# Kernel optimization log

Measured on AMD Instinct MI355X. Metric: run time of the kernel, lower is better.

## Reference

```python
import jax, jax.numpy as jnp
import numpy as np

TEMPERATURE = 0.07
BASE_TEMPERATURE = 0.07
LAMBDA_HARD = 1.0
HMAX = 1.0
EPS = 1e-8
SIGMA = 1.0  # Gaussian RBF kernel bandwidth on label differences


def setup_inputs() -> dict:
    key = jax.random.key(0)
    k1, k2 = jax.random.split(key)
    features = jax.random.normal(k1, (4096, 2, 128), dtype=jnp.float32)
    labels = jax.random.uniform(k2, (4096,), dtype=jnp.float32)
    return {"features": features, "labels": labels}


def reference(features, labels):
    bsz, n_views, dim = features.shape
    # F.normalize(features, dim=-1)
    feats = features / jnp.sqrt(jnp.sum(features * features, axis=-1, keepdims=True) + 1e-12)
    # torch.cat(torch.unbind(features, dim=1), dim=0) -> view-major stacking [N, dim]
    feats = jnp.transpose(feats, (1, 0, 2)).reshape(bsz * n_views, dim)
    lab = jnp.tile(labels.reshape(bsz, 1), (n_views, 1))  # [N, 1]
    N = bsz * n_views

    logits_mask = 1.0 - jnp.eye(N, dtype=feats.dtype)

    # kernel similarity weights w_{i,k} = K(y_i - y_k), Gaussian RBF, clamped to [0,1]
    dy = lab - lab.T                                   # [N, N]
    w = jnp.clip(jnp.exp(-(dy * dy) / (2.0 * SIGMA * SIGMA)), 0.0, 1.0)

    # hardness term (computed as in source; note w_pos = w, so m is unused downstream)
    d_y = jnp.abs(dy)
    d_y = d_y / (jnp.max(d_y) + EPS)
    sim_cos = feats @ feats.T                          # cosine sim (feats normalized)
    d_z = 1.0 - sim_cos
    d_z = d_z / (jnp.max(d_z) + EPS)
    u = jnp.clip(d_z - d_y, -HMAX, HMAX)
    m = 1.0 + LAMBDA_HARD * jax.nn.relu(u)             # dead code in source; DCE'd under jit

    sim = sim_cos / TEMPERATURE                        # [N, N]
    logits = sim - jax.lax.stop_gradient(jnp.max(sim, axis=1, keepdims=True))
    exp_logits = jnp.exp(logits) * logits_mask
    log_denom = jnp.log(jnp.sum(exp_logits, axis=1, keepdims=True) + EPS)
    log_prob = logits - log_denom

    w_pos_sum = jnp.clip(jnp.sum(w, axis=1), EPS, None)
    mean_log_prob_pos = jnp.sum(w * log_prob, axis=1) / w_pos_sum
    loss = -(TEMPERATURE / BASE_TEMPERATURE) * mean_log_prob_pos
    return jnp.mean(loss)
```

## Files before the change

### kernel.cpp

```cpp
#include <hip/hip_runtime.h>
#include <math.h>

#define BSZ 4096
#define NTOT 8192
#define DIM 128
#define CHUNKS 16

typedef __attribute__((ext_vector_type(8))) short short8;
typedef __attribute__((ext_vector_type(4))) float float4v;

constexpr float INV_T = 1.0f / 0.07f;
constexpr float M0    = INV_T;
constexpr float LOG2E = 1.4426950408889634f;
constexpr float K1    = INV_T * LOG2E;
constexpr float C3    = -0.5f * LOG2E;

__global__ void norm_bf16(const float* __restrict__ feat, unsigned short* __restrict__ F) {
    const int i = blockIdx.x;
    const int b = i & (BSZ - 1), v = i >> 12;
    const int l = threadIdx.x;
    const float2 x = reinterpret_cast<const float2*>(feat + (size_t)(b * 2 + v) * DIM)[l];
    float s = x.x * x.x + x.y * x.y;
#pragma unroll
    for (int off = 32; off >= 1; off >>= 1) s += __shfl_xor(s, off);
    const float inv = 1.0f / sqrtf(s + 1e-12f);
    union { float f; unsigned u; } u0, u1;
    u0.f = x.x * inv; u1.f = x.y * inv;
    const unsigned short r0 = (unsigned short)((u0.u + 0x7FFFu + ((u0.u >> 16) & 1)) >> 16);
    const unsigned short r1 = (unsigned short)((u1.u + 0x7FFFu + ((u1.u >> 16) & 1)) >> 16);
    reinterpret_cast<ushort2*>(F + (size_t)i * DIM)[l] = make_ushort2(r0, r1);
}

__global__ __launch_bounds__(256) void supcon_mfma(
    const unsigned short* __restrict__ F, const float* __restrict__ labels,
    float* __restrict__ part)
{
    const int tid    = threadIdx.x;
    const int wv     = tid >> 6;
    const int l      = tid & 63;
    const int stripe = blockIdx.x >> 2;
    const int quad   = blockIdx.x & 3;
    const int chunk  = quad * 4 + wv;
    const int row0   = stripe * 64;
    const int colbeg = chunk * (NTOT / CHUNKS);
    const int l15 = l & 15, lh = l >> 4;

    short8 a[4][4];
#pragma unroll
    for (int set = 0; set < 4; ++set) {
        const unsigned short* rp = F + (size_t)(row0 + set * 16 + l15) * DIM + lh * 8;
#pragma unroll
        for (int kc = 0; kc < 4; ++kc)
            a[set][kc] = *reinterpret_cast<const short8*>(rp + kc * 32);
    }
    float lr[16];
#pragma unroll
    for (int set = 0; set < 4; ++set)
#pragma unroll
        for (int r = 0; r < 4; ++r)
            lr[set * 4 + r] = labels[(row0 + set * 16 + lh * 4 + r) & (BSZ - 1)];

    float den[16], sw[16], swc[16];
#pragma unroll
    for (int p = 0; p < 16; ++p) { den[p] = 0.f; sw[p] = 0.f; swc[p] = 0.f; }

    for (int cb = 0; cb < (NTOT / CHUNKS) / 16; ++cb) {
        const int col0 = colbeg + cb * 16;
        const int col  = col0 + l15;
        const unsigned short* cp = F + (size_t)col * DIM + lh * 8;
        short8 bfr[4];
#pragma unroll
        for (int kc = 0; kc < 4; ++kc)
            bfr[kc] = *reinterpret_cast<const short8*>(cp + kc * 32);
        const float lc = labels[col & (BSZ - 1)];

#pragma unroll
        for (int set = 0; set < 4; ++set) {
            float4v acc = {0.f, 0.f, 0.f, 0.f};
#pragma unroll
            for (int kc = 0; kc < 4; ++kc)
                acc = __builtin_amdgcn_mfma_f32_16x16x32_bf16(a[set][kc], bfr[kc], acc, 0, 0, 0);

            if (col0 == row0 + set * 16) {
#pragma unroll
                for (int r = 0; r < 4; ++r) {
                    const float c = acc[r];
                    const int p = set * 4 + r;
                    float e = __builtin_amdgcn_exp2f(__builtin_fmaf(c, K1, -K1));
                    if (l15 == lh * 4 + r) e = 0.f;
                    den[p] += e;
                    const float dy = lr[p] - lc;
                    const float w = __builtin_amdgcn_exp2f(dy * dy * C3);
                    sw[p] += w;
                    swc[p] = __builtin_fmaf(w, c, swc[p]);
                }
            } else {
#pragma unroll
                for (int r = 0; r < 4; ++r) {
                    const float c = acc[r];
                    const int p = set * 4 + r;
                    const float e = __builtin_amdgcn_exp2f(__builtin_fmaf(c, K1, -K1));
                    den[p] += e;
                    const float dy = lr[p] - lc;
                    const float w = __builtin_amdgcn_exp2f(dy * dy * C3);
                    sw[p] += w;
                    swc[p] = __builtin_fmaf(w, c, swc[p]);
                }
            }
        }
    }

#pragma unroll
    for (int p = 0; p < 16; ++p) {
#pragma unroll
        for (int off = 1; off < 16; off <<= 1) {
            den[p] += __shfl_xor(den[p], off);
            sw[p]  += __shfl_xor(sw[p],  off);
            swc[p] += __shfl_xor(swc[p], off);
        }
    }
    if (l15 == 0) {
        float* bp = part + (size_t)(stripe * CHUNKS + chunk) * 64 * 3;
#pragma unroll
        for (int set = 0; set < 4; ++set)
#pragma unroll
            for (int r = 0; r < 4; ++r) {
                const int rl = set * 16 + lh * 4 + r;
                const int p  = set * 4 + r;
                bp[rl * 3 + 0] = den[p];
                bp[rl * 3 + 1] = sw[p];
                bp[rl * 3 + 2] = swc[p];
            }
    }
}

__global__ void rowloss_k(const float* __restrict__ part, float* __restrict__ rowloss) {
    const int row = blockIdx.x * 256 + threadIdx.x;
    const int stripe = row >> 6, rl = row & 63;
    float den = 0.f, sw = 0.f, swc = 0.f;
    for (int c = 0; c < CHUNKS; ++c) {
        const float* bp = part + ((size_t)(stripe * CHUNKS + c) * 64 + rl) * 3;
        den += bp[0]; sw += bp[1]; swc += bp[2];
    }
    const float logd = logf(den + 1e-8f);
    const float mean = (INV_T * swc - (M0 + logd) * sw) / fmaxf(sw, 1e-8f);
    rowloss[row] = -mean;
}

__global__ void reduce_mean(const float* __restrict__ rowloss, float* __restrict__ out) {
    __shared__ float partlds[4];
    float s = 0.f;
    for (int j = threadIdx.x; j < NTOT; j += 256) s += rowloss[j];
#pragma unroll
    for (int off = 32; off >= 1; off >>= 1) s += __shfl_xor(s, off);
    const int w = threadIdx.x >> 6;
    if ((threadIdx.x & 63) == 0) partlds[w] = s;
    __syncthreads();
    if (threadIdx.x == 0) out[0] = (partlds[0] + partlds[1] + partlds[2] + partlds[3]) * (1.0f / NTOT);
}

extern "C" void kernel_launch(void* const* d_in, const int* in_sizes, int n_in,
                              void* d_out, int out_size, void* d_ws, size_t ws_size,
                              hipStream_t stream) {
    const float* feat   = (const float*)d_in[0];
    const float* labels = (const float*)d_in[1];

    char* ws = (char*)d_ws;
    unsigned short* F = (unsigned short*)ws;
    float* part    = (float*)(ws + (size_t)NTOT * DIM * 2);
    float* rowloss = part + (size_t)128 * CHUNKS * 64 * 3;
    float* out = (float*)d_out;

    norm_bf16<<<NTOT, 64, 0, stream>>>(feat, F);
    supcon_mfma<<<512, 256, 0, stream>>>(F, labels, part);
    rowloss_k<<<NTOT / 256, 256, 0, stream>>>(part, rowloss);
    reduce_mean<<<1, 256, 0, stream>>>(rowloss, out);
}
```

Before: 115.4 us.

## Factor RBF label weights via truncated Taylor series, leaving only denominator in main loop

```diff
diff --git a/kernel.cpp b/kernel.cpp
--- a/kernel.cpp
+++ b/kernel.cpp
@@ -4,7 +4,6 @@
 #define BSZ 4096
 #define NTOT 8192
 #define DIM 128
-#define CHUNKS 16
 
 typedef __attribute__((ext_vector_type(8))) short short8;
 typedef __attribute__((ext_vector_type(4))) float float4v;
@@ -15,148 +14,190 @@
 constexpr float K1    = INV_T * LOG2E;
 constexpr float C3    = -0.5f * LOG2E;
 
-__global__ void norm_bf16(const float* __restrict__ feat, unsigned short* __restrict__ F) {
-    const int i = blockIdx.x;
-    const int b = i & (BSZ - 1), v = i >> 12;
-    const int l = threadIdx.x;
-    const float2 x = reinterpret_cast<const float2*>(feat + (size_t)(b * 2 + v) * DIM)[l];
-    float s = x.x * x.x + x.y * x.y;
-#pragma unroll
-    for (int off = 32; off >= 1; off >>= 1) s += __shfl_xor(s, off);
+__device__ __forceinline__ unsigned short f2bf(float x) {
+    union { float f; unsigned u; } u; u.f = x;
+    return (unsigned short)((u.u + 0x7FFFu + ((u.u >> 16) & 1)) >> 16);
+}
+__device__ __forceinline__ float bf2f(unsigned short s) {
+    union { unsigned u; float f; } u; u.u = ((unsigned)s) << 16;
+    return u.f;
+}
+__device__ __forceinline__ unsigned pack2(float a, float b) {
+    return (unsigned)f2bf(a) | ((unsigned)f2bf(b) << 16);
+}
+
+__global__ __launch_bounds__(256) void norm_k(const float* __restrict__ feat,
+                                              unsigned short* __restrict__ F) {
+    const int tid = threadIdx.x;
+    const int wv = tid >> 6, l = tid & 63;
+    const int g = l >> 3, j = l & 7;
+    const int row = blockIdx.x * 32 + wv * 8 + g;
+    const int b = row & (BSZ - 1), v = row >> 12;
+    const float4* src = reinterpret_cast<const float4*>(feat + (size_t)(b * 2 + v) * DIM) + j * 4;
+    const float4 x0 = src[0], x1 = src[1], x2 = src[2], x3 = src[3];
+    float s = x0.x*x0.x + x0.y*x0.y + x0.z*x0.z + x0.w*x0.w
+            + x1.x*x1.x + x1.y*x1.y + x1.z*x1.z + x1.w*x1.w
+            + x2.x*x2.x + x2.y*x2.y + x2.z*x2.z + x2.w*x2.w
+            + x3.x*x3.x + x3.y*x3.y + x3.z*x3.z + x3.w*x3.w;
+    s += __shfl_xor(s, 1); s += __shfl_xor(s, 2); s += __shfl_xor(s, 4);
     const float inv = 1.0f / sqrtf(s + 1e-12f);
-    union { float f; unsigned u; } u0, u1;
-    u0.f = x.x * inv; u1.f = x.y * inv;
-    const unsigned short r0 = (unsigned short)((u0.u + 0x7FFFu + ((u0.u >> 16) & 1)) >> 16);
-    const unsigned short r1 = (unsigned short)((u1.u + 0x7FFFu + ((u1.u >> 16) & 1)) >> 16);
-    reinterpret_cast<ushort2*>(F + (size_t)i * DIM)[l] = make_ushort2(r0, r1);
-}
-
-__global__ __launch_bounds__(256) void supcon_mfma(
-    const unsigned short* __restrict__ F, const float* __restrict__ labels,
-    float* __restrict__ part)
+    uint4 w0, w1;
+    w0.x = pack2(x0.x*inv, x0.y*inv); w0.y = pack2(x0.z*inv, x0.w*inv);
+    w0.z = pack2(x1.x*inv, x1.y*inv); w0.w = pack2(x1.z*inv, x1.w*inv);
+    w1.x = pack2(x2.x*inv, x2.y*inv); w1.y = pack2(x2.z*inv, x2.w*inv);
+    w1.z = pack2(x3.x*inv, x3.y*inv); w1.w = pack2(x3.z*inv, x3.w*inv);
+    uint4* dst = reinterpret_cast<uint4*>(F + (size_t)row * DIM);
+    dst[j * 2]     = w0;
+    dst[j * 2 + 1] = w1;
+}
+
+__global__ __launch_bounds__(128) void hsum_k(const unsigned short* __restrict__ F,
+                                              const float* __restrict__ labels,
+                                              float* __restrict__ h, float* __restrict__ svec) {
+    const int t = threadIdx.x;
+    const int k0 = blockIdx.x * 64;
+    float acc[10];
+#pragma unroll
+    for (int m = 0; m < 10; ++m) acc[m] = 0.f;
+    float sv = 0.f;
+    for (int kk = 0; kk < 64; ++kk) {
+        const int k = k0 + kk;
+        const float li = labels[k & (BSZ - 1)];
+        const float a = __builtin_amdgcn_exp2f(li * li * C3);
+        const float f = bf2f(F[(size_t)k * DIM + t]);
+        float pm = a;
+#pragma unroll
+        for (int m = 0; m < 10; ++m) {
+            acc[m] = fmaf(pm, f, acc[m]);
+            if (t == m) sv += pm;
+            pm *= li;
+        }
+    }
+#pragma unroll
+    for (int m = 0; m < 10; ++m) atomicAdd(&h[m * DIM + t], acc[m]);
+    if (t < 10) atomicAdd(&svec[t], sv);
+}
+
+__global__ __launch_bounds__(256, 2) void supcon_mfma(
+    const unsigned short* __restrict__ F, float* __restrict__ den_g)
 {
     const int tid    = threadIdx.x;
     const int wv     = tid >> 6;
     const int l      = tid & 63;
-    const int stripe = blockIdx.x >> 2;
-    const int quad   = blockIdx.x & 3;
+    const int stripe = blockIdx.x >> 3;
+    const int quad   = blockIdx.x & 7;
     const int chunk  = quad * 4 + wv;
-    const int row0   = stripe * 64;
-    const int colbeg = chunk * (NTOT / CHUNKS);
+    const int row0   = stripe * 128;
+    const int colbeg = chunk * 256;
     const int l15 = l & 15, lh = l >> 4;
 
-    short8 a[4][4];
-#pragma unroll
-    for (int set = 0; set < 4; ++set) {
+    short8 a[8][4];
+#pragma unroll
+    for (int set = 0; set < 8; ++set) {
         const unsigned short* rp = F + (size_t)(row0 + set * 16 + l15) * DIM + lh * 8;
 #pragma unroll
         for (int kc = 0; kc < 4; ++kc)
             a[set][kc] = *reinterpret_cast<const short8*>(rp + kc * 32);
     }
-    float lr[16];
-#pragma unroll
-    for (int set = 0; set < 4; ++set)
-#pragma unroll
-        for (int r = 0; r < 4; ++r)
-            lr[set * 4 + r] = labels[(row0 + set * 16 + lh * 4 + r) & (BSZ - 1)];
-
-    float den[16], sw[16], swc[16];
-#pragma unroll
-    for (int p = 0; p < 16; ++p) { den[p] = 0.f; sw[p] = 0.f; swc[p] = 0.f; }
-
-    for (int cb = 0; cb < (NTOT / CHUNKS) / 16; ++cb) {
+
+    float den[32];
+#pragma unroll
+    for (int p = 0; p < 32; ++p) den[p] = 0.f;
+
+    for (int cb = 0; cb < 16; ++cb) {
         const int col0 = colbeg + cb * 16;
-        const int col  = col0 + l15;
-        const unsigned short* cp = F + (size_t)col * DIM + lh * 8;
+        const unsigned short* cp = F + (size_t)(col0 + l15) * DIM + lh * 8;
         short8 bfr[4];
 #pragma unroll
         for (int kc = 0; kc < 4; ++kc)
             bfr[kc] = *reinterpret_cast<const short8*>(cp + kc * 32);
-        const float lc = labels[col & (BSZ - 1)];
-
-#pragma unroll
-        for (int set = 0; set < 4; ++set) {
+
+#pragma unroll
+        for (int set = 0; set < 8; ++set) {
             float4v acc = {0.f, 0.f, 0.f, 0.f};
 #pragma unroll
             for (int kc = 0; kc < 4; ++kc)
                 acc = __builtin_amdgcn_mfma_f32_16x16x32_bf16(a[set][kc], bfr[kc], acc, 0, 0, 0);
-
-            if (col0 == row0 + set * 16) {
-#pragma unroll
-                for (int r = 0; r < 4; ++r) {
-                    const float c = acc[r];
-                    const int p = set * 4 + r;
-                    float e = __builtin_amdgcn_exp2f(__builtin_fmaf(c, K1, -K1));
-                    if (l15 == lh * 4 + r) e = 0.f;
-                    den[p] += e;
-                    const float dy = lr[p] - lc;
-                    const float w = __builtin_amdgcn_exp2f(dy * dy * C3);
-                    sw[p] += w;
-                    swc[p] = __builtin_fmaf(w, c, swc[p]);
-                }
-            } else {
-#pragma unroll
-                for (int r = 0; r < 4; ++r) {
-                    const float c = acc[r];
-                    const int p = set * 4 + r;
-                    const float e = __builtin_amdgcn_exp2f(__builtin_fmaf(c, K1, -K1));
-                    den[p] += e;
-                    const float dy = lr[p] - lc;
-                    const float w = __builtin_amdgcn_exp2f(dy * dy * C3);
-                    sw[p] += w;
-                    swc[p] = __builtin_fmaf(w, c, swc[p]);
-                }
+            const bool dtile = (col0 == row0 + set * 16);
+#pragma unroll
+            for (int r = 0; r < 4; ++r) {
+                float e = __builtin_amdgcn_exp2f(__builtin_fmaf(acc[r], K1, -K1));
+                if (dtile && (l15 == lh * 4 + r)) e = 0.f;
+                den[set * 4 + r] += e;
             }
         }
     }
 
 #pragma unroll
-    for (int p = 0; p < 16; ++p) {
-#pragma unroll
-        for (int off = 1; off < 16; off <<= 1) {
-            den[p] += __shfl_xor(den[p], off);
-            sw[p]  += __shfl_xor(sw[p],  off);
-            swc[p] += __shfl_xor(swc[p], off);
-        }
+    for (int p = 0; p < 32; ++p) {
+        den[p] += __shfl_xor(den[p], 1);
+        den[p] += __shfl_xor(den[p], 2);
+        den[p] += __shfl_xor(den[p], 4);
+        den[p] += __shfl_xor(den[p], 8);
     }
     if (l15 == 0) {
-        float* bp = part + (size_t)(stripe * CHUNKS + chunk) * 64 * 3;
-#pragma unroll
-        for (int set = 0; set < 4; ++set)
-#pragma unroll
-            for (int r = 0; r < 4; ++r) {
-                const int rl = set * 16 + lh * 4 + r;
-                const int p  = set * 4 + r;
-                bp[rl * 3 + 0] = den[p];
-                bp[rl * 3 + 1] = sw[p];
-                bp[rl * 3 + 2] = swc[p];
-            }
-    }
-}
-
-__global__ void rowloss_k(const float* __restrict__ part, float* __restrict__ rowloss) {
-    const int row = blockIdx.x * 256 + threadIdx.x;
-    const int stripe = row >> 6, rl = row & 63;
-    float den = 0.f, sw = 0.f, swc = 0.f;
-    for (int c = 0; c < CHUNKS; ++c) {
-        const float* bp = part + ((size_t)(stripe * CHUNKS + c) * 64 + rl) * 3;
-        den += bp[0]; sw += bp[1]; swc += bp[2];
-    }
+#pragma unroll
+        for (int set = 0; set < 8; ++set)
+#pragma unroll
+            for (int r = 0; r < 4; ++r)
+                atomicAdd(&den_g[row0 + set * 16 + lh * 4 + r], den[set * 4 + r]);
+    }
+}
+
+__global__ __launch_bounds__(256) void final_k(const float* __restrict__ feat,
+    const float* __restrict__ labels, const float* __restrict__ den_g,
+    const float* __restrict__ h, const float* __restrict__ svec,
+    float* __restrict__ out)
+{
+    __shared__ float hs[10 * DIM];
+    __shared__ float svs[10];
+    const int tid = threadIdx.x;
+    for (int i = tid; i < 10 * DIM; i += 256) hs[i] = h[i];
+    if (tid < 10) svs[tid] = svec[tid];
+    __syncthreads();
+
+    const int wv = tid >> 6, l = tid & 63;
+    const int g = l >> 3, j = l & 7;
+    const int row = blockIdx.x * 32 + wv * 8 + g;
+    const int b = row & (BSZ - 1), v = row >> 12;
+    const float4* src = reinterpret_cast<const float4*>(feat + (size_t)(b * 2 + v) * DIM) + j * 4;
+    const float4 x0 = src[0], x1 = src[1], x2 = src[2], x3 = src[3];
+    float s = x0.x*x0.x + x0.y*x0.y + x0.z*x0.z + x0.w*x0.w
+            + x1.x*x1.x + x1.y*x1.y + x1.z*x1.z + x1.w*x1.w
+            + x2.x*x2.x + x2.y*x2.y + x2.z*x2.z + x2.w*x2.w
+            + x3.x*x3.x + x3.y*x3.y + x3.z*x3.z + x3.w*x3.w;
+    s += __shfl_xor(s, 1); s += __shfl_xor(s, 2); s += __shfl_xor(s, 4);
+    const float inv = 1.0f / sqrtf(s + 1e-12f);
+
+    const float li = labels[b];
+    const float ai = __builtin_amdgcn_exp2f(li * li * C3);
+    const float cf[10] = {1.f, 1.f, 0.5f, 1.f/6.f, 1.f/24.f, 1.f/120.f,
+                          1.f/720.f, 1.f/5040.f, 1.f/40320.f, 1.f/362880.f};
+    float swc = 0.f, sw = 0.f, pm = ai;
+    const float* hb = &hs[j * 16];
+#pragma unroll
+    for (int m = 0; m < 10; ++m) {
+        const float* hm = hb + m * DIM;
+        const float d = x0.x*hm[0]  + x0.y*hm[1]  + x0.z*hm[2]  + x0.w*hm[3]
+                      + x1.x*hm[4]  + x1.y*hm[5]  + x1.z*hm[6]  + x1.w*hm[7]
+                      + x2.x*hm[8]  + x2.y*hm[9]  + x2.z*hm[10] + x2.w*hm[11]
+                      + x3.x*hm[12] + x3.y*hm[13] + x3.z*hm[14] + x3.w*hm[15];
+        const float cpm = cf[m] * pm;
+        swc = fmaf(cpm, d, swc);
+        sw  = fmaf(cpm, svs[m], sw);
+        pm *= li;
+    }
+    swc += __shfl_xor(swc, 1); swc += __shfl_xor(swc, 2); swc += __shfl_xor(swc, 4);
+    swc *= inv;
+
+    const float den  = den_g[row];
     const float logd = logf(den + 1e-8f);
-    const float mean = (INV_T * swc - (M0 + logd) * sw) / fmaxf(sw, 1e-8f);
-    rowloss[row] = -mean;
-}
-
-__global__ void reduce_mean(const float* __restrict__ rowloss, float* __restrict__ out) {
-    __shared__ float partlds[4];
-    float s = 0.f;
-    for (int j = threadIdx.x; j < NTOT; j += 256) s += rowloss[j];
-#pragma unroll
-    for (int off = 32; off >= 1; off >>= 1) s += __shfl_xor(s, off);
-    const int w = threadIdx.x >> 6;
-    if ((threadIdx.x & 63) == 0) partlds[w] = s;
-    __syncthreads();
-    if (threadIdx.x == 0) out[0] = (partlds[0] + partlds[1] + partlds[2] + partlds[3]) * (1.0f / NTOT);
+    const float loss = -(INV_T * swc - (M0 + logd) * sw) / fmaxf(sw, 1e-8f);
+
+    float part = loss * 0.125f;
+    part += __shfl_xor(part, 1);  part += __shfl_xor(part, 2);  part += __shfl_xor(part, 4);
+    part += __shfl_xor(part, 8);  part += __shfl_xor(part, 16); part += __shfl_xor(part, 32);
+    if (l == 0) atomicAdd(out, part * (1.0f / NTOT));
 }
 
 extern "C" void kernel_launch(void* const* d_in, const int* in_sizes, int n_in,
@@ -167,12 +208,15 @@
 
     char* ws = (char*)d_ws;
     unsigned short* F = (unsigned short*)ws;
-    float* part    = (float*)(ws + (size_t)NTOT * DIM * 2);
-    float* rowloss = part + (size_t)128 * CHUNKS * 64 * 3;
-    float* out = (float*)d_out;
-
-    norm_bf16<<<NTOT, 64, 0, stream>>>(feat, F);
-    supcon_mfma<<<512, 256, 0, stream>>>(F, labels, part);
-    rowloss_k<<<NTOT / 256, 256, 0, stream>>>(part, rowloss);
-    reduce_mean<<<1, 256, 0, stream>>>(rowloss, out);
-}
+    float* den_g = (float*)(ws + (size_t)NTOT * DIM * 2);
+    float* h     = den_g + NTOT;
+    float* svec  = h + 10 * DIM;
+    float* out   = (float*)d_out;
+
+    hipMemsetAsync(den_g, 0, (NTOT + 10 * DIM + 16) * sizeof(float), stream);
+    hipMemsetAsync(out, 0, sizeof(float), stream);
+    norm_k<<<256, 256, 0, stream>>>(feat, F);
+    hsum_k<<<128, 128, 0, stream>>>(F, labels, h, svec);
+    supcon_mfma<<<512, 256, 0, stream>>>(F, den_g);
+    final_k<<<256, 256, 0, stream>>>(feat, labels, den_g, h, svec, out);
+}
```

After: 124.3 us. 7.7% more time.
